# Kernel tuning notes

Hardware: AMD Instinct MI355X
Metric: run time of the kernel (lower is better)

The kernel has to match this reference:

```python
import jax, jax.numpy as jnp
import numpy as np

B, N, D = 8, 2048, 256

def setup_inputs() -> dict:
    key = jax.random.key(0)
    ks = jax.random.split(key, 8)
    sc = 1.0 / np.sqrt(D)
    return {
        "x": jax.random.normal(ks[0], (B, N, D), dtype=jnp.float32),
        "W_fp": jax.random.normal(ks[1], (D, D), dtype=jnp.float32) * sc,
        "b_fp": jnp.zeros((D,), dtype=jnp.float32),
        "w_s": jax.random.normal(ks[2], (D,), dtype=jnp.float32) * sc,
        "b_s": jnp.zeros((), dtype=jnp.float32),
        "W_rp": jax.random.normal(ks[3], (D, D), dtype=jnp.float32) * sc,
        "b_rp": jnp.zeros((D,), dtype=jnp.float32),
        "W_gp": jax.random.normal(ks[4], (D, D), dtype=jnp.float32) * sc,
        "b_gp": jnp.zeros((D,), dtype=jnp.float32),
        "gamma": jnp.ones((D,), dtype=jnp.float32),
        "beta": jnp.zeros((D,), dtype=jnp.float32),
    }

def reference(x, W_fp, b_fp, w_s, b_s, W_rp, b_rp, W_gp, b_gp, gamma, beta):
    # feature projection: [B, N, D]
    proj = jnp.einsum('bnd,de->bne', x, W_fp) + b_fp
    # F.normalize(p=2, dim=-1) with eps=1e-12
    nrm = jnp.sqrt(jnp.sum(proj * proj, axis=-1, keepdims=True))
    xn = proj / jnp.maximum(nrm, 1e-12)
    # cosine similarity matrix [B, N, N]
    sim = jnp.einsum('bnd,bmd->bnm', xn, xn)
    # adj_scaler: Linear(D,1)+sigmoid is constant along the broadcast axis ->
    # compute per-node scalar once [B, N] (same math as the O(N^2*D) expand)
    s = jax.nn.sigmoid(jnp.einsum('bnd,d->bn', proj, w_s) + b_s)
    scaler = jnp.clip(0.5 * (s[:, :, None] + s[:, None, :]), 1e-6, 1.0)
    adj = jnp.maximum(scaler * sim, 1e-6)  # clamp(min=1e-6)
    degree = jnp.maximum(jnp.sum(adj, axis=2, keepdims=True), 1e-6)
    norm_adj = adj / degree
    # aggregation + region projection
    region = jnp.einsum('bnm,bmd->bnd', norm_adj, proj)
    region = jnp.einsum('bnd,de->bne', region, W_rp) + b_rp
    # global pooling + projection: [B, 1, D]
    g = jnp.mean(region, axis=1, keepdims=True)
    g = jnp.einsum('bnd,de->bne', g, W_gp) + b_gp
    input_global = jnp.mean(x, axis=1, keepdims=True)
    h = g + input_global
    # LayerNorm (eps=1e-5)
    mu = jnp.mean(h, axis=-1, keepdims=True)
    var = jnp.mean((h - mu) ** 2, axis=-1, keepdims=True)
    out = (h - mu) / jnp.sqrt(var + 1e-5) * gamma + beta
    return out, adj
```

## Files before the change

kernel.cpp:

```cpp
#include <hip/hip_runtime.h>
#include <hip/hip_bf16.h>
#include <math.h>

#define Bn 8
#define Nn 2048
#define Dn 256

typedef short short8 __attribute__((ext_vector_type(8)));
typedef float floatx4 __attribute__((ext_vector_type(4)));

__device__ __forceinline__ short f2bf_bits(float f) {
    __bf16 h = (__bf16)f;
    return __builtin_bit_cast(short, h);
}

__device__ __forceinline__ float bf2f(short s) {
    unsigned u = ((unsigned)(unsigned short)s) << 16;
    return __builtin_bit_cast(float, u);
}

__device__ __forceinline__ void gl_lds16(const void* gsrc, void* ldst) {
    __builtin_amdgcn_global_load_lds(
        (const __attribute__((address_space(1))) void*)gsrc,
        (__attribute__((address_space(3))) void*)ldst, 16, 0, 0);
}

__device__ __forceinline__ float sigmoidf_(float z) {
    return 1.0f / (1.0f + __expf(-z));
}


__global__ void k_transpose(const float* __restrict__ W, short* __restrict__ Wt) {
    int e = blockIdx.x, d = threadIdx.x;
    Wt[e * Dn + d] = f2bf_bits(W[d * Dn + e]);
}


__global__ __launch_bounds__(256) void k_projxn(
    const float* __restrict__ x, const short* __restrict__ Wt,
    const float* __restrict__ b_fp, const float* __restrict__ w_s,
    short* __restrict__ xn, float* __restrict__ sdot, float* __restrict__ nrm,
    float* __restrict__ xpart) {
    __shared__ __align__(16) short As[64 * 64];
    __shared__ __align__(16) short Bs[256 * 64];
    __shared__ float xsumS[4 * 256];
    const int t = threadIdx.x;
    const int bm = blockIdx.x * 64;
    const int lane = t & 63, wv = t >> 6;
    const int wm = wv * 16;
    const int l15 = lane & 15, q = lane >> 4;

    for (int i = t; i < 1024; i += 256) xsumS[i] = 0.f;

    floatx4 acc[16];
    #pragma unroll
    for (int j = 0; j < 16; ++j) acc[j] = (floatx4){0.f, 0.f, 0.f, 0.f};

    const int rA = t >> 2, cA = (t & 3) * 16;
    const int rB = t >> 3, cB = (t & 7) * 8;

    for (int k0 = 0; k0 < Dn; k0 += 64) {
        const float* gp = x + (size_t)(bm + rA) * Dn + k0 + cA;
        float4 v0 = *(const float4*)gp;
        float4 v1 = *(const float4*)(gp + 4);
        float4 v2 = *(const float4*)(gp + 8);
        float4 v3 = *(const float4*)(gp + 12);
        short8 o0, o1;
        o0[0] = f2bf_bits(v0.x); o0[1] = f2bf_bits(v0.y);
        o0[2] = f2bf_bits(v0.z); o0[3] = f2bf_bits(v0.w);
        o0[4] = f2bf_bits(v1.x); o0[5] = f2bf_bits(v1.y);
        o0[6] = f2bf_bits(v1.z); o0[7] = f2bf_bits(v1.w);
        o1[0] = f2bf_bits(v2.x); o1[1] = f2bf_bits(v2.y);
        o1[2] = f2bf_bits(v2.z); o1[3] = f2bf_bits(v2.w);
        o1[4] = f2bf_bits(v3.x); o1[5] = f2bf_bits(v3.y);
        o1[6] = f2bf_bits(v3.z); o1[7] = f2bf_bits(v3.w);
        *(short8*)(As + rA * 64 + cA) = o0;
        *(short8*)(As + rA * 64 + cA + 8) = o1;
        #pragma unroll
        for (int cc = 0; cc < 8; ++cc)
            gl_lds16(Wt + (size_t)(cc * 32 + rB) * Dn + k0 + cB,
                     Bs + (cc * 32 + rB) * 64 + cB);
        __syncthreads();
        #pragma unroll
        for (int ks = 0; ks < 2; ++ks) {
            short8 af = *(const short8*)(As + (wm + l15) * 64 + ks * 32 + q * 8);
            #pragma unroll
            for (int j = 0; j < 16; ++j) {
                short8 bfr = *(const short8*)(Bs + (j * 16 + l15) * 64 + ks * 32 + q * 8);
                acc[j] = __builtin_amdgcn_mfma_f32_16x16x32_bf16(af, bfr, acc[j], 0, 0, 0);
            }
        }
        {
            float s = 0.f;
            #pragma unroll
            for (int r = 0; r < 16; ++r)
                s += bf2f(As[(wm + r) * 64 + lane]);
            xsumS[wv * 256 + k0 + lane] += s;
        }
        __syncthreads();
    }
    {
        float xs = xsumS[t] + xsumS[256 + t] + xsumS[512 + t] + xsumS[768 + t];
        xpart[(size_t)blockIdx.x * Dn + t] = xs;
    }
    float bfv[16], wsv[16];
    #pragma unroll
    for (int j = 0; j < 16; ++j) {
        bfv[j] = b_fp[j * 16 + l15];
        wsv[j] = w_s[j * 16 + l15];
    }
    #pragma unroll
    for (int reg = 0; reg < 4; ++reg) {
        int row = bm + wm + q * 4 + reg;
        float v[16];
        float pw = 0.f, pn = 0.f;
        #pragma unroll
        for (int j = 0; j < 16; ++j) {
            v[j] = acc[j][reg] + bfv[j];
            pw += v[j] * wsv[j];
            pn += v[j] * v[j];
        }
        #pragma unroll
        for (int m = 1; m < 16; m <<= 1) {
            pw += __shfl_xor(pw, m);
            pn += __shfl_xor(pn, m);
        }
        float nc = fmaxf(sqrtf(pn), 1e-12f);
        float inv = 1.0f / nc;
        size_t rbase = (size_t)row * Dn + l15;
        #pragma unroll
        for (int j = 0; j < 16; ++j)
            xn[rbase + j * 16] = f2bf_bits(v[j] * inv);
        if (l15 == 0) {
            sdot[row] = pw;
            nrm[row] = nc;
        }
    }
}


__global__ __launch_bounds__(256) void k_sim(
    const short* __restrict__ xn, const float* __restrict__ sdot,
    const float* __restrict__ b_s, float* __restrict__ adj,
    float* __restrict__ deg_part) {
    __shared__ __align__(16) short As[128 * 64];
    __shared__ __align__(16) short Bs[128 * 64];
    __shared__ float degS[2][128];
    const int t = threadIdx.x;
    int lin = (blockIdx.z * 16 + blockIdx.y) * 16 + blockIdx.x;
    const int b = lin & 7;
    const int pos = lin >> 3;
    const int by = pos >> 4, cx = pos & 15;
    const int bn = cx * 128;
    const int bm = by * 128;
    const int lane = t & 63, wv = t >> 6;
    const int wm = (wv >> 1) * 64, wn = (wv & 1) * 64;
    const int l15 = lane & 15, q4 = lane >> 4;
    const int rr = t >> 3, c8 = (t & 7) * 8;
    const short* xb = xn + (size_t)b * Nn * Dn;

    floatx4 acc[4][4];
    #pragma unroll
    for (int i = 0; i < 4; ++i)
        #pragma unroll
        for (int j = 0; j < 4; ++j) acc[i][j] = (floatx4){0.f, 0.f, 0.f, 0.f};

    for (int k0 = 0; k0 < Dn; k0 += 64) {
        #pragma unroll
        for (int cc = 0; cc < 4; ++cc) {
            int r = cc * 32 + rr;
            gl_lds16(xb + (size_t)(bm + r) * Dn + k0 + c8, As + r * 64 + c8);
            gl_lds16(xb + (size_t)(bn + r) * Dn + k0 + c8, Bs + r * 64 + c8);
        }
        __syncthreads();
        #pragma unroll
        for (int ks = 0; ks < 2; ++ks) {
            short8 af[4], bfr[4];
            #pragma unroll
            for (int i = 0; i < 4; ++i)
                af[i] = *(const short8*)(As + (wm + i * 16 + l15) * 64 + ks * 32 + q4 * 8);
            #pragma unroll
            for (int j = 0; j < 4; ++j)
                bfr[j] = *(const short8*)(Bs + (wn + j * 16 + l15) * 64 + ks * 32 + q4 * 8);
            #pragma unroll
            for (int i = 0; i < 4; ++i)
                #pragma unroll
                for (int j = 0; j < 4; ++j)
                    acc[i][j] = __builtin_amdgcn_mfma_f32_16x16x32_bf16(bfr[j], af[i], acc[i][j], 0, 0, 0);
        }
        __syncthreads();
    }
    const float bsv = b_s[0];
    float srow[4];
    #pragma unroll
    for (int i = 0; i < 4; ++i)
        srow[i] = sigmoidf_(sdot[b * Nn + bm + wm + i * 16 + l15] + bsv);
    float scol[4][4];
    #pragma unroll
    for (int j = 0; j < 4; ++j)
        #pragma unroll
        for (int reg = 0; reg < 4; ++reg)
            scol[j][reg] = sigmoidf_(sdot[b * Nn + bn + wn + j * 16 + q4 * 4 + reg] + bsv);
    #pragma unroll
    for (int i = 0; i < 4; ++i) {
        float rs = 0.f;
        size_t rbase = ((size_t)b * Nn + (bm + wm + i * 16 + l15)) * Nn + bn + wn + q4 * 4;
        #pragma unroll
        for (int j = 0; j < 4; ++j) {
            float4 o;
            float sc;
            sc = fminf(fmaxf(0.5f * (srow[i] + scol[j][0]), 1e-6f), 1.0f);
            o.x = fmaxf(sc * acc[i][j][0], 1e-6f);
            sc = fminf(fmaxf(0.5f * (srow[i] + scol[j][1]), 1e-6f), 1.0f);
            o.y = fmaxf(sc * acc[i][j][1], 1e-6f);
            sc = fminf(fmaxf(0.5f * (srow[i] + scol[j][2]), 1e-6f), 1.0f);
            o.z = fmaxf(sc * acc[i][j][2], 1e-6f);
            sc = fminf(fmaxf(0.5f * (srow[i] + scol[j][3]), 1e-6f), 1.0f);
            o.w = fmaxf(sc * acc[i][j][3], 1e-6f);
            *(float4*)(adj + rbase + (size_t)j * 16) = o;
            rs += o.x + o.y + o.z + o.w;
        }
        rs += __shfl_xor(rs, 16);
        rs += __shfl_xor(rs, 32);
        if (q4 == 0) degS[wv & 1][wm + i * 16 + l15] = rs;
    }
    __syncthreads();
    if (t < 128)
        deg_part[((size_t)(b * 16 + cx)) * Nn + bm + t] = degS[0][t] + degS[1][t];
}


__global__ __launch_bounds__(512) void k_colsum(
    const float* __restrict__ adj, const float* __restrict__ deg_part,
    const short* __restrict__ xn, const float* __restrict__ nrm,
    float* __restrict__ gpart) {
    int b = blockIdx.x, ck = blockIdx.y, t = threadIdx.x;
    __shared__ float invdeg[Nn];
    __shared__ float part[32][64];
    __shared__ float csL[64];
    __shared__ float gHalf[2][Dn];
    #pragma unroll
    for (int rc = 0; rc < 4; ++rc) {
        int row = rc * 512 + t;
        float s = 0.f;
        #pragma unroll
        for (int cx = 0; cx < 16; ++cx)
            s += deg_part[((size_t)(b * 16 + cx)) * Nn + row];
        invdeg[row] = 1.0f / fmaxf(s, 1e-6f);
    }
    __syncthreads();
    const int lc = (t & 15) * 4;
    const int rg = t >> 4;
    const int c0 = ck * 64;
    float sx = 0.f, sy = 0.f, sz = 0.f, sw = 0.f;
    for (int r = rg; r < Nn; r += 32) {
        float4 v = *(const float4*)(adj + ((size_t)b * Nn + r) * Nn + c0 + lc);
        float w = invdeg[r];
        sx += v.x * w; sy += v.y * w; sz += v.z * w; sw += v.w * w;
    }
    part[rg][lc + 0] = sx; part[rg][lc + 1] = sy;
    part[rg][lc + 2] = sz; part[rg][lc + 3] = sw;
    __syncthreads();
    if (t < 64) {
        float s = 0.f;
        #pragma unroll
        for (int g = 0; g < 32; ++g) s += part[g][t];
        csL[t] = s * nrm[b * Nn + c0 + t];
    }
    __syncthreads();
    {
        int h = t >> 8, d = t & 255;
        float g = 0.f;
        #pragma unroll 4
        for (int mi = 0; mi < 32; ++mi) {
            int m = h * 32 + mi;
            g += csL[m] * bf2f(xn[((size_t)(b * Nn + c0 + m)) * Dn + d]);
        }
        gHalf[h][d] = g;
    }
    __syncthreads();
    if (t < Dn)
        gpart[(b * 32 + ck) * Dn + t] = gHalf[0][t] + gHalf[1][t];
}


__global__ __launch_bounds__(256) void k_final2(
    const float* __restrict__ gpart, const float* __restrict__ xpart,
    const float* __restrict__ W_rp, const float* __restrict__ b_rp,
    const float* __restrict__ W_gp, const float* __restrict__ b_gp,
    const float* __restrict__ gamma, const float* __restrict__ beta,
    float* __restrict__ out) {
    int b = blockIdx.x, t = threadIdx.x;
    __shared__ float gp_s[Dn];
    __shared__ float g1_s[Dn];
    __shared__ float red[8];
    float gs = 0.f, xs = 0.f;
    #pragma unroll
    for (int ck = 0; ck < 32; ++ck) {
        gs += gpart[(b * 32 + ck) * Dn + t];
        xs += xpart[(b * 32 + ck) * Dn + t];
    }
    gp_s[t] = gs * (1.0f / Nn);
    float xm = xs * (1.0f / Nn);
    __syncthreads();
    float g1 = b_rp[t];
    #pragma unroll 4
    for (int d = 0; d < Dn; ++d) g1 += gp_s[d] * W_rp[d * Dn + t];
    g1_s[t] = g1;
    __syncthreads();
    float g2 = b_gp[t];
    #pragma unroll 4
    for (int e = 0; e < Dn; ++e) g2 += g1_s[e] * W_gp[e * Dn + t];
    float h = g2 + xm;
    float sum = h;
    #pragma unroll
    for (int m = 1; m < 64; m <<= 1) sum += __shfl_xor(sum, m);
    if ((t & 63) == 0) red[t >> 6] = sum;
    __syncthreads();
    float mu = (red[0] + red[1] + red[2] + red[3]) * (1.0f / Dn);
    float dv = h - mu;
    float s2 = dv * dv;
    #pragma unroll
    for (int m = 1; m < 64; m <<= 1) s2 += __shfl_xor(s2, m);
    if ((t & 63) == 0) red[4 + (t >> 6)] = s2;
    __syncthreads();
    float var = (red[4] + red[5] + red[6] + red[7]) * (1.0f / Dn);
    out[b * Dn + t] = dv * rsqrtf(var + 1e-5f) * gamma[t] + beta[t];
}


extern "C" void kernel_launch(void* const* d_in, const int* in_sizes, int n_in,
                              void* d_out, int out_size, void* d_ws, size_t ws_size,
                              hipStream_t stream) {
    const float* x     = (const float*)d_in[0];
    const float* W_fp  = (const float*)d_in[1];
    const float* b_fp  = (const float*)d_in[2];
    const float* w_s   = (const float*)d_in[3];
    const float* b_s   = (const float*)d_in[4];
    const float* W_rp  = (const float*)d_in[5];
    const float* b_rp  = (const float*)d_in[6];
    const float* W_gp  = (const float*)d_in[7];
    const float* b_gp  = (const float*)d_in[8];
    const float* gamma = (const float*)d_in[9];
    const float* beta  = (const float*)d_in[10];

    float* out = (float*)d_out;
    float* adj = out + Bn * Dn;

    char* ws = (char*)d_ws;
    short* xn    = (short*)(ws);
    short* Wt    = (short*)(ws + 8388608);
    float* sdot  = (float*)(ws + 8519680);
    float* nrm   = (float*)(ws + 8585216);
    float* degp  = (float*)(ws + 8650752);
    float* gpart = (float*)(ws + 9699328);
    float* xpart = (float*)(ws + 9961472);

    k_transpose<<<Dn, Dn, 0, stream>>>(W_fp, Wt);
    k_projxn<<<(Bn * Nn) / 64, 256, 0, stream>>>(x, Wt, b_fp, w_s, xn, sdot, nrm, xpart);
    k_sim<<<dim3(Nn / 128, Nn / 128, Bn), 256, 0, stream>>>(xn, sdot, b_s, adj, degp);
    k_colsum<<<dim3(Bn, 32), 512, 0, stream>>>(adj, degp, xn, nrm, gpart);
    k_final2<<<Bn, 256, 0, stream>>>(gpart, xpart, W_rp, b_rp, W_gp, b_gp, gamma, beta, out);
}
```

Measured before the change: 280.3 us.

## Widen blocks in projection, colsum and final kernels; tile the weight transpose

The weight transpose becomes a shared-memory tiled 64x64 kernel with vectorised bf16 stores, replacing a 256-block strided scatter. The projection kernel moves to 512 threads, splitting the 256 output columns across two wave groups and combining row norms and score dots through shared memory. The column-sum and final LayerNorm kernels move to 1024 threads, spreading the row reduction and the two small GEMVs across four thread groups. The aim is more parallelism and latency hiding in the small kernels that run around the dominant similarity kernel, at the cost of extra barriers and shared-memory reductions.

Result: faster. 238.4 us (-15.0%).

```diff
diff --git a/kernel.cpp b/kernel.cpp
--- a/kernel.cpp
+++ b/kernel.cpp
@@ -30,108 +30,138 @@
 }
 
 
-__global__ void k_transpose(const float* __restrict__ W, short* __restrict__ Wt) {
-    int e = blockIdx.x, d = threadIdx.x;
-    Wt[e * Dn + d] = f2bf_bits(W[d * Dn + e]);
-}
-
-
-__global__ __launch_bounds__(256) void k_projxn(
+__global__ __launch_bounds__(256) void k_transpose(const float* __restrict__ W,
+                                                   short* __restrict__ Wt) {
+    __shared__ float Ts[64][65];
+    const int t = threadIdx.x;
+    const int dt0 = blockIdx.x * 64, et0 = blockIdx.y * 64;
+    const int ro = t >> 4, co = (t & 15) * 4;
+    #pragma unroll
+    for (int rr = 0; rr < 4; ++rr) {
+        int row = rr * 16 + ro;
+        float4 v = *(const float4*)(W + (size_t)(dt0 + row) * Dn + et0 + co);
+        Ts[row][co + 0] = v.x; Ts[row][co + 1] = v.y;
+        Ts[row][co + 2] = v.z; Ts[row][co + 3] = v.w;
+    }
+    __syncthreads();
+    const int e = t >> 2, cd0 = (t & 3) * 16;
+    short8 a, b;
+    #pragma unroll
+    for (int i = 0; i < 8; ++i) {
+        a[i] = f2bf_bits(Ts[cd0 + i][e]);
+        b[i] = f2bf_bits(Ts[cd0 + 8 + i][e]);
+    }
+    *(short8*)(Wt + (size_t)(et0 + e) * Dn + dt0 + cd0) = a;
+    *(short8*)(Wt + (size_t)(et0 + e) * Dn + dt0 + cd0 + 8) = b;
+}
+
+
+__global__ __launch_bounds__(512) void k_projxn(
     const float* __restrict__ x, const short* __restrict__ Wt,
     const float* __restrict__ b_fp, const float* __restrict__ w_s,
     short* __restrict__ xn, float* __restrict__ sdot, float* __restrict__ nrm,
     float* __restrict__ xpart) {
     __shared__ __align__(16) short As[64 * 64];
     __shared__ __align__(16) short Bs[256 * 64];
-    __shared__ float xsumS[4 * 256];
+    __shared__ float xsumS[8 * 256];
+    __shared__ float redW[2][64];
+    __shared__ float redN[2][64];
     const int t = threadIdx.x;
     const int bm = blockIdx.x * 64;
     const int lane = t & 63, wv = t >> 6;
-    const int wm = wv * 16;
+    const int wm = (wv & 3) * 16;
+    const int jh = wv >> 2;
     const int l15 = lane & 15, q = lane >> 4;
 
-    for (int i = t; i < 1024; i += 256) xsumS[i] = 0.f;
-
-    floatx4 acc[16];
-    #pragma unroll
-    for (int j = 0; j < 16; ++j) acc[j] = (floatx4){0.f, 0.f, 0.f, 0.f};
-
-    const int rA = t >> 2, cA = (t & 3) * 16;
+    for (int i = t; i < 2048; i += 512) xsumS[i] = 0.f;
+
+    floatx4 acc[8];
+    #pragma unroll
+    for (int j = 0; j < 8; ++j) acc[j] = (floatx4){0.f, 0.f, 0.f, 0.f};
+
+    const int rA = t >> 3, cA = (t & 7) * 8;
     const int rB = t >> 3, cB = (t & 7) * 8;
 
     for (int k0 = 0; k0 < Dn; k0 += 64) {
         const float* gp = x + (size_t)(bm + rA) * Dn + k0 + cA;
         float4 v0 = *(const float4*)gp;
         float4 v1 = *(const float4*)(gp + 4);
-        float4 v2 = *(const float4*)(gp + 8);
-        float4 v3 = *(const float4*)(gp + 12);
-        short8 o0, o1;
+        short8 o0;
         o0[0] = f2bf_bits(v0.x); o0[1] = f2bf_bits(v0.y);
         o0[2] = f2bf_bits(v0.z); o0[3] = f2bf_bits(v0.w);
         o0[4] = f2bf_bits(v1.x); o0[5] = f2bf_bits(v1.y);
         o0[6] = f2bf_bits(v1.z); o0[7] = f2bf_bits(v1.w);
-        o1[0] = f2bf_bits(v2.x); o1[1] = f2bf_bits(v2.y);
-        o1[2] = f2bf_bits(v2.z); o1[3] = f2bf_bits(v2.w);
-        o1[4] = f2bf_bits(v3.x); o1[5] = f2bf_bits(v3.y);
-        o1[6] = f2bf_bits(v3.z); o1[7] = f2bf_bits(v3.w);
         *(short8*)(As + rA * 64 + cA) = o0;
-        *(short8*)(As + rA * 64 + cA + 8) = o1;
-        #pragma unroll
-        for (int cc = 0; cc < 8; ++cc)
-            gl_lds16(Wt + (size_t)(cc * 32 + rB) * Dn + k0 + cB,
-                     Bs + (cc * 32 + rB) * 64 + cB);
+        #pragma unroll
+        for (int cc = 0; cc < 4; ++cc)
+            gl_lds16(Wt + (size_t)(cc * 64 + rB) * Dn + k0 + cB,
+                     Bs + (cc * 64 + rB) * 64 + cB);
         __syncthreads();
         #pragma unroll
         for (int ks = 0; ks < 2; ++ks) {
             short8 af = *(const short8*)(As + (wm + l15) * 64 + ks * 32 + q * 8);
             #pragma unroll
-            for (int j = 0; j < 16; ++j) {
-                short8 bfr = *(const short8*)(Bs + (j * 16 + l15) * 64 + ks * 32 + q * 8);
-                acc[j] = __builtin_amdgcn_mfma_f32_16x16x32_bf16(af, bfr, acc[j], 0, 0, 0);
+            for (int jj = 0; jj < 8; ++jj) {
+                short8 bfr = *(const short8*)(Bs + (jh * 128 + jj * 16 + l15) * 64 + ks * 32 + q * 8);
+                acc[jj] = __builtin_amdgcn_mfma_f32_16x16x32_bf16(af, bfr, acc[jj], 0, 0, 0);
             }
         }
         {
             float s = 0.f;
             #pragma unroll
-            for (int r = 0; r < 16; ++r)
-                s += bf2f(As[(wm + r) * 64 + lane]);
+            for (int r = 0; r < 8; ++r)
+                s += bf2f(As[(wv * 8 + r) * 64 + lane]);
             xsumS[wv * 256 + k0 + lane] += s;
         }
         __syncthreads();
     }
-    {
-        float xs = xsumS[t] + xsumS[256 + t] + xsumS[512 + t] + xsumS[768 + t];
+    if (t < 256) {
+        float xs = 0.f;
+        #pragma unroll
+        for (int w = 0; w < 8; ++w) xs += xsumS[w * 256 + t];
         xpart[(size_t)blockIdx.x * Dn + t] = xs;
     }
-    float bfv[16], wsv[16];
-    #pragma unroll
-    for (int j = 0; j < 16; ++j) {
-        bfv[j] = b_fp[j * 16 + l15];
-        wsv[j] = w_s[j * 16 + l15];
-    }
+    float bfv[8], wsv[8];
+    #pragma unroll
+    for (int jj = 0; jj < 8; ++jj) {
+        bfv[jj] = b_fp[jh * 128 + jj * 16 + l15];
+        wsv[jj] = w_s[jh * 128 + jj * 16 + l15];
+    }
+    float vv[4][8];
     #pragma unroll
     for (int reg = 0; reg < 4; ++reg) {
-        int row = bm + wm + q * 4 + reg;
-        float v[16];
         float pw = 0.f, pn = 0.f;
         #pragma unroll
-        for (int j = 0; j < 16; ++j) {
-            v[j] = acc[j][reg] + bfv[j];
-            pw += v[j] * wsv[j];
-            pn += v[j] * v[j];
+        for (int jj = 0; jj < 8; ++jj) {
+            float v = acc[jj][reg] + bfv[jj];
+            vv[reg][jj] = v;
+            pw += v * wsv[jj];
+            pn += v * v;
         }
         #pragma unroll
         for (int m = 1; m < 16; m <<= 1) {
             pw += __shfl_xor(pw, m);
             pn += __shfl_xor(pn, m);
         }
+        if (l15 == 0) {
+            redW[jh][wm + q * 4 + reg] = pw;
+            redN[jh][wm + q * 4 + reg] = pn;
+        }
+    }
+    __syncthreads();
+    #pragma unroll
+    for (int reg = 0; reg < 4; ++reg) {
+        int lr = wm + q * 4 + reg;
+        float pw = redW[0][lr] + redW[1][lr];
+        float pn = redN[0][lr] + redN[1][lr];
         float nc = fmaxf(sqrtf(pn), 1e-12f);
         float inv = 1.0f / nc;
-        size_t rbase = (size_t)row * Dn + l15;
-        #pragma unroll
-        for (int j = 0; j < 16; ++j)
-            xn[rbase + j * 16] = f2bf_bits(v[j] * inv);
-        if (l15 == 0) {
+        int row = bm + lr;
+        size_t rbase = (size_t)row * Dn + jh * 128 + l15;
+        #pragma unroll
+        for (int jj = 0; jj < 8; ++jj)
+            xn[rbase + jj * 16] = f2bf_bits(vv[reg][jj] * inv);
+        if (jh == 0 && l15 == 0) {
             sdot[row] = pw;
             nrm[row] = nc;
         }
@@ -230,18 +260,18 @@
 }
 
 
-__global__ __launch_bounds__(512) void k_colsum(
+__global__ __launch_bounds__(1024) void k_colsum(
     const float* __restrict__ adj, const float* __restrict__ deg_part,
     const short* __restrict__ xn, const float* __restrict__ nrm,
     float* __restrict__ gpart) {
     int b = blockIdx.x, ck = blockIdx.y, t = threadIdx.x;
     __shared__ float invdeg[Nn];
-    __shared__ float part[32][64];
+    __shared__ float part[64][64];
     __shared__ float csL[64];
-    __shared__ float gHalf[2][Dn];
-    #pragma unroll
-    for (int rc = 0; rc < 4; ++rc) {
-        int row = rc * 512 + t;
+    __shared__ float gQ[4][Dn];
+    #pragma unroll
+    for (int rc = 0; rc < 2; ++rc) {
+        int row = rc * 1024 + t;
         float s = 0.f;
         #pragma unroll
         for (int cx = 0; cx < 16; ++cx)
@@ -253,7 +283,7 @@
     const int rg = t >> 4;
     const int c0 = ck * 64;
     float sx = 0.f, sy = 0.f, sz = 0.f, sw = 0.f;
-    for (int r = rg; r < Nn; r += 32) {
+    for (int r = rg; r < Nn; r += 64) {
         float4 v = *(const float4*)(adj + ((size_t)b * Nn + r) * Nn + c0 + lc);
         float w = invdeg[r];
         sx += v.x * w; sy += v.y * w; sz += v.z * w; sw += v.w * w;
@@ -264,7 +294,7 @@
     if (t < 64) {
         float s = 0.f;
         #pragma unroll
-        for (int g = 0; g < 32; ++g) s += part[g][t];
+        for (int g = 0; g < 64; ++g) s += part[g][t];
         csL[t] = s * nrm[b * Nn + c0 + t];
     }
     __syncthreads();
@@ -272,60 +302,94 @@
         int h = t >> 8, d = t & 255;
         float g = 0.f;
         #pragma unroll 4
-        for (int mi = 0; mi < 32; ++mi) {
-            int m = h * 32 + mi;
+        for (int mi = 0; mi < 16; ++mi) {
+            int m = h * 16 + mi;
             g += csL[m] * bf2f(xn[((size_t)(b * Nn + c0 + m)) * Dn + d]);
         }
-        gHalf[h][d] = g;
+        gQ[h][d] = g;
     }
     __syncthreads();
     if (t < Dn)
-        gpart[(b * 32 + ck) * Dn + t] = gHalf[0][t] + gHalf[1][t];
-}
-
-
-__global__ __launch_bounds__(256) void k_final2(
+        gpart[(b * 32 + ck) * Dn + t] = gQ[0][t] + gQ[1][t] + gQ[2][t] + gQ[3][t];
+}
+
+
+__global__ __launch_bounds__(1024) void k_final2(
     const float* __restrict__ gpart, const float* __restrict__ xpart,
     const float* __restrict__ W_rp, const float* __restrict__ b_rp,
     const float* __restrict__ W_gp, const float* __restrict__ b_gp,
     const float* __restrict__ gamma, const float* __restrict__ beta,
     float* __restrict__ out) {
     int b = blockIdx.x, t = threadIdx.x;
+    const int d = t & 255, c4 = t >> 8;
+    __shared__ float pS[4][Dn];
+    __shared__ float xS[4][Dn];
     __shared__ float gp_s[Dn];
+    __shared__ float xm_s[Dn];
     __shared__ float g1_s[Dn];
     __shared__ float red[8];
-    float gs = 0.f, xs = 0.f;
-    #pragma unroll
-    for (int ck = 0; ck < 32; ++ck) {
-        gs += gpart[(b * 32 + ck) * Dn + t];
-        xs += xpart[(b * 32 + ck) * Dn + t];
-    }
-    gp_s[t] = gs * (1.0f / Nn);
-    float xm = xs * (1.0f / Nn);
-    __syncthreads();
-    float g1 = b_rp[t];
-    #pragma unroll 4
-    for (int d = 0; d < Dn; ++d) g1 += gp_s[d] * W_rp[d * Dn + t];
-    g1_s[t] = g1;
-    __syncthreads();
-    float g2 = b_gp[t];
-    #pragma unroll 4
-    for (int e = 0; e < Dn; ++e) g2 += g1_s[e] * W_gp[e * Dn + t];
-    float h = g2 + xm;
-    float sum = h;
-    #pragma unroll
-    for (int m = 1; m < 64; m <<= 1) sum += __shfl_xor(sum, m);
-    if ((t & 63) == 0) red[t >> 6] = sum;
+    {
+        float gs = 0.f, xs = 0.f;
+        #pragma unroll
+        for (int k = 0; k < 8; ++k) {
+            int ck = c4 * 8 + k;
+            gs += gpart[(b * 32 + ck) * Dn + d];
+            xs += xpart[(b * 32 + ck) * Dn + d];
+        }
+        pS[c4][d] = gs;
+        xS[c4][d] = xs;
+    }
+    __syncthreads();
+    if (t < Dn) {
+        gp_s[t] = (pS[0][t] + pS[1][t] + pS[2][t] + pS[3][t]) * (1.0f / Nn);
+        xm_s[t] = (xS[0][t] + xS[1][t] + xS[2][t] + xS[3][t]) * (1.0f / Nn);
+    }
+    __syncthreads();
+    {
+        float m1 = 0.f;
+        #pragma unroll 4
+        for (int i = 0; i < 64; ++i) {
+            int dd = c4 * 64 + i;
+            m1 += gp_s[dd] * W_rp[dd * Dn + d];
+        }
+        pS[c4][d] = m1;
+    }
+    __syncthreads();
+    if (t < Dn) g1_s[t] = b_rp[t] + pS[0][t] + pS[1][t] + pS[2][t] + pS[3][t];
+    __syncthreads();
+    {
+        float m2 = 0.f;
+        #pragma unroll 4
+        for (int i = 0; i < 64; ++i) {
+            int ee = c4 * 64 + i;
+            m2 += g1_s[ee] * W_gp[ee * Dn + d];
+        }
+        pS[c4][d] = m2;
+    }
+    __syncthreads();
+    float h = 0.f;
+    if (t < Dn) {
+        h = b_gp[t] + pS[0][t] + pS[1][t] + pS[2][t] + pS[3][t] + xm_s[t];
+        float sum = h;
+        #pragma unroll
+        for (int m = 1; m < 64; m <<= 1) sum += __shfl_xor(sum, m);
+        if ((t & 63) == 0) red[t >> 6] = sum;
+    }
     __syncthreads();
     float mu = (red[0] + red[1] + red[2] + red[3]) * (1.0f / Dn);
-    float dv = h - mu;
-    float s2 = dv * dv;
-    #pragma unroll
-    for (int m = 1; m < 64; m <<= 1) s2 += __shfl_xor(s2, m);
-    if ((t & 63) == 0) red[4 + (t >> 6)] = s2;
-    __syncthreads();
-    float var = (red[4] + red[5] + red[6] + red[7]) * (1.0f / Dn);
-    out[b * Dn + t] = dv * rsqrtf(var + 1e-5f) * gamma[t] + beta[t];
+    if (t < Dn) {
+        float dv = h - mu;
+        float s2 = dv * dv;
+        #pragma unroll
+        for (int m = 1; m < 64; m <<= 1) s2 += __shfl_xor(s2, m);
+        if ((t & 63) == 0) red[4 + (t >> 6)] = s2;
+    }
+    __syncthreads();
+    if (t < Dn) {
+        float dv = h - mu;
+        float var = (red[4] + red[5] + red[6] + red[7]) * (1.0f / Dn);
+        out[b * Dn + t] = dv * rsqrtf(var + 1e-5f) * gamma[t] + beta[t];
+    }
 }
 
 
@@ -356,9 +420,9 @@
     float* gpart = (float*)(ws + 9699328);
     float* xpart = (float*)(ws + 9961472);
 
-    k_transpose<<<Dn, Dn, 0, stream>>>(W_fp, Wt);
-    k_projxn<<<(Bn * Nn) / 64, 256, 0, stream>>>(x, Wt, b_fp, w_s, xn, sdot, nrm, xpart);
+    k_transpose<<<dim3(4, 4), 256, 0, stream>>>(W_fp, Wt);
+    k_projxn<<<(Bn * Nn) / 64, 512, 0, stream>>>(x, Wt, b_fp, w_s, xn, sdot, nrm, xpart);
     k_sim<<<dim3(Nn / 128, Nn / 128, Bn), 256, 0, stream>>>(xn, sdot, b_s, adj, degp);
-    k_colsum<<<dim3(Bn, 32), 512, 0, stream>>>(adj, degp, xn, nrm, gpart);
-    k_final2<<<Bn, 256, 0, stream>>>(gpart, xpart, W_rp, b_rp, W_gp, b_gp, gamma, beta, out);
-}
+    k_colsum<<<dim3(Bn, 32), 1024, 0, stream>>>(adj, degp, xn, nrm, gpart);
+    k_final2<<<Bn, 1024, 0, stream>>>(gpart, xpart, W_rp, b_rp, W_gp, b_gp, gamma, beta, out);
+}
```
